# Kernel optimization log

Hardware: AMD Instinct MI355X
Metric: run time of the kernel (lower is better)

Reference implementation:

```python
import jax, jax.numpy as jnp
import numpy as np
import itertools

RANK = 2  # window size per axis; mode='linear' -> stride 1; rank_op='avg'; rank_mode='drop'


def setup_inputs() -> dict:
    key = jax.random.key(0)
    k1, k2, k3 = jax.random.split(key, 3)
    m = 32
    D = 20
    hypervol = jax.random.normal(k1, (D, D, D, D, m), dtype=jnp.float32)
    # nn.Linear weight init U(-0.5, 0.5); P init U(-0.1, 0.1)
    M_w = jax.random.uniform(k2, (m, m), dtype=jnp.float32, minval=-0.5, maxval=0.5)
    P = jax.random.uniform(k3, (m, m), dtype=jnp.float32, minval=-0.1, maxval=0.1)
    return {"hypervol": hypervol, "M_w": M_w, "P": P}


def reference(hypervol, M_w, P):
    m = P.shape[0]
    D1, D2, D3, D4, _ = hypervol.shape
    o1, o2, o3, o4 = D1 - RANK + 1, D2 - RANK + 1, D3 - RANK + 1, D4 - RANK + 1

    # Vectorized window extraction with mean reduction ('avg'):
    # mean over RANK^4 window = average of RANK^4 shifted slices (fixed small loop).
    acc = jnp.zeros((o1, o2, o3, o4, m), dtype=hypervol.dtype)
    for a, b, c, d in itertools.product(range(RANK), repeat=4):
        acc = acc + hypervol[a:a + o1, b:b + o2, c:c + o3, d:d + o4, :]
    win = acc / float(RANK ** 4)  # [o1,o2,o3,o4,m]

    # M(v): Linear without bias -> v @ W^T
    x = jnp.einsum('abcdj,ij->abcdi', win, M_w)  # [o1,o2,o3,o4,m]
    # note: output index of Linear is i; below x plays role of (M v) with einsum index j
    x = jnp.einsum('abcdi->abcdi', x)  # no-op, keep shape clear

    # periods[i,j] = i*m + j + 2 (identical for all four axes)
    ii = jnp.arange(m, dtype=jnp.float32)
    periods = ii[:, None] * m + ii[None, :] + 2.0  # [m,m]
    two_pi = jnp.float32(2.0 * np.pi)

    def ctab(n):
        k = jnp.arange(n, dtype=jnp.float32)
        return jnp.cos(two_pi * k[:, None, None] / periods)  # [n,m,m]

    C1, C2, C3, C4 = ctab(o1), ctab(o2), ctab(o3), ctab(o4)
    # phi[a,b,c,d,i,j] = C1[a]*C2[b]*C3[c]*C4[d]; built from tiny per-axis tables
    phi = (C1[:, None, None, None] * C2[None, :, None, None]) \
          [:, :, :, None] * 0.0  # placeholder removed below
    phi = (C1[:, None, None, None, :, :]
           * C2[None, :, None, None, :, :]
           * C3[None, None, :, None, :, :]
           * C4[None, None, None, :, :, :])  # [o1,o2,o3,o4,m,m]

    # N(k)_i = sum_j P_ij * (Mv)_j * phi_ij  (matches einsum 'bj,ij,bij->bi')
    Nk = jnp.einsum('abcdj,ij,abcdij->abcdi', x, P, phi)
    return Nk.reshape(-1, m)  # [num_windows, m], window order = k1-major like the loops
```

## Files before the change

kernel.cpp:

```cpp
#include <hip/hip_runtime.h>

#define DD 20
#define MM 32
#define OO 19
#define NBLK (OO*OO*OO)

#define CT_FLOATS (OO*MM*MM)
#define PT_OFF CT_FLOATS
#define MT_OFF (PT_OFF + MM*MM)
#define WS_FLOATS (MT_OFF + MM*MM)

__global__ __launch_bounds__(256) void build_tables_kernel(
        const float* __restrict__ Mw, const float* __restrict__ P,
        float* __restrict__ ws) {
    int idx = blockIdx.x * 256 + threadIdx.x;
    if (idx < CT_FLOATS) {
        int k = idx >> 10;
        int r = idx & 1023;
        int j = r >> 5;
        int i = r & 31;
        float period = (float)(i * MM + j + 2);
        ws[idx] = cosf(6.28318530717958647692f * (float)k / period);
    } else if (idx < MT_OFF) {
        int r = idx - PT_OFF;
        ws[idx] = P[(r & 31) * MM + (r >> 5)];
    } else if (idx < WS_FLOATS) {
        int r = idx - MT_OFF;
        ws[idx] = Mw[(r & 31) * MM + (r >> 5)];
    }
}

__global__ __launch_bounds__(256) void spatial_kernel(
        const float* __restrict__ H, const float* __restrict__ ws,
        float* __restrict__ out) {
    __shared__ float sS[DD * MM];
    __shared__ float sMt[MM * MM];
    __shared__ float sQPt[MM * MM];
    __shared__ float sX[OO * MM];

    const int tid = threadIdx.x;
    const int i = tid & 31;
    const int g = tid >> 5;

    const int blk = blockIdx.x;
    const int c = blk % OO;
    const int b = (blk / OO) % OO;
    const int a = blk / (OO * OO);

    const float* __restrict__ Ct = ws;
    const float* __restrict__ Pt = ws + PT_OFF;
    const float* __restrict__ Mt = ws + MT_OFF;

    ((float4*)sMt)[tid] = ((const float4*)Mt)[tid];

    {
        float4 p  = ((const float4*)Pt)[tid];
        float4 xa = ((const float4*)(Ct + a * (MM*MM)))[tid];
        float4 xb = ((const float4*)(Ct + b * (MM*MM)))[tid];
        float4 xc = ((const float4*)(Ct + c * (MM*MM)))[tid];
        float4 q;
        q.x = p.x * xa.x * xb.x * xc.x;
        q.y = p.y * xa.y * xb.y * xc.y;
        q.z = p.z * xa.z * xb.z * xc.z;
        q.w = p.w * xa.w * xb.w * xc.w;
        ((float4*)sQPt)[tid] = q;
    }

    for (int d = g; d < DD; d += 8) {
        float s = 0.f;
        #pragma unroll
        for (int da = 0; da < 2; ++da)
            #pragma unroll
            for (int db = 0; db < 2; ++db)
                #pragma unroll
                for (int dc = 0; dc < 2; ++dc) {
                    int base = (((a + da) * DD + (b + db)) * DD + (c + dc)) * DD + d;
                    s += H[base * MM + i];
                }
        sS[d * MM + i] = s;
    }
    __syncthreads();

    for (int d = g; d < OO; d += 8) {
        float acc = 0.f;
        #pragma unroll
        for (int j = 0; j < MM; ++j) {
            float wj = (sS[d * MM + j] + sS[(d + 1) * MM + j]) * 0.0625f;
            acc += wj * sMt[j * MM + i];
        }
        sX[d * MM + i] = acc;
    }
    __syncthreads();

    for (int d = g; d < OO; d += 8) {
        float xr[MM];
        #pragma unroll
        for (int jj = 0; jj < MM / 4; ++jj) {
            float4 v = ((const float4*)(sX + d * MM))[jj];
            xr[jj*4+0] = v.x; xr[jj*4+1] = v.y; xr[jj*4+2] = v.z; xr[jj*4+3] = v.w;
        }
        const float* __restrict__ ctd = Ct + d * (MM*MM) + i;
        float acc = 0.f;
        #pragma unroll
        for (int j = 0; j < MM; ++j) {
            acc += xr[j] * sQPt[j * MM + i] * ctd[j * MM];
        }
        out[(blk * OO + d) * MM + i] = acc;
    }
}

extern "C" void kernel_launch(void* const* d_in, const int* in_sizes, int n_in,
                              void* d_out, int out_size, void* d_ws, size_t ws_size,
                              hipStream_t stream) {
    const float* H  = (const float*)d_in[0];
    const float* Mw = (const float*)d_in[1];
    const float* P  = (const float*)d_in[2];
    float* out = (float*)d_out;
    float* ws  = (float*)d_ws;

    const int tblocks = (WS_FLOATS + 255) / 256;
    build_tables_kernel<<<tblocks, 256, 0, stream>>>(Mw, P, ws);
    spatial_kernel<<<NBLK, 256, 0, stream>>>(H, ws, out);
}
```

Measured before the change: 112.8 us.

## Register-tile two outputs per thread, vectorize loads, and remap blocks per XCD

Each thread now computes two output channels across a contiguous range of d rows. The per-block P·Ca·Cb·Cc product is held in registers as float2 instead of shared memory. Window sums use float4 loads from H, the averaged row is staged once in a padded shared buffer, and block IDs are remapped so neighbouring blocks land on the same XCD for better L2 reuse of overlapping H slices. The trade is higher register pressure (64 floats for qp plus 32 for xr) and an uneven d split across thread groups (2 rows for g<3, 1 otherwise).

```diff
diff --git a/kernel.cpp b/kernel.cpp
--- a/kernel.cpp
+++ b/kernel.cpp
@@ -9,6 +9,8 @@
 #define PT_OFF CT_FLOATS
 #define MT_OFF (PT_OFF + MM*MM)
 #define WS_FLOATS (MT_OFF + MM*MM)
+
+#define SWS 36
 
 __global__ __launch_bounds__(256) void build_tables_kernel(
         const float* __restrict__ Mw, const float* __restrict__ P,
@@ -34,15 +36,21 @@
         const float* __restrict__ H, const float* __restrict__ ws,
         float* __restrict__ out) {
     __shared__ float sS[DD * MM];
+    __shared__ float sW[OO * SWS];
+    __shared__ float sX[OO * SWS];
     __shared__ float sMt[MM * MM];
-    __shared__ float sQPt[MM * MM];
-    __shared__ float sX[OO * MM];
 
     const int tid = threadIdx.x;
-    const int i = tid & 31;
-    const int g = tid >> 5;
+    const int i2  = tid & 15;
+    const int i   = i2 * 2;
+    const int g   = tid >> 4;
+    const int d0  = (g < 3) ? (2 * g) : (g + 3);
+    const int d1  = d0 + ((g < 3) ? 2 : 1);
 
-    const int blk = blockIdx.x;
+    const int raw = blockIdx.x;
+    const int xcd = raw & 7;
+    const int k   = raw >> 3;
+    const int blk = (xcd < 3) ? (xcd * 858 + k) : (2574 + (xcd - 3) * 857 + k);
     const int c = blk % OO;
     const int b = (blk / OO) % OO;
     const int a = blk / (OO * OO);
@@ -53,59 +61,80 @@
 
     ((float4*)sMt)[tid] = ((const float4*)Mt)[tid];
 
+    float2 qp[MM];
     {
-        float4 p  = ((const float4*)Pt)[tid];
-        float4 xa = ((const float4*)(Ct + a * (MM*MM)))[tid];
-        float4 xb = ((const float4*)(Ct + b * (MM*MM)))[tid];
-        float4 xc = ((const float4*)(Ct + c * (MM*MM)))[tid];
-        float4 q;
-        q.x = p.x * xa.x * xb.x * xc.x;
-        q.y = p.y * xa.y * xb.y * xc.y;
-        q.z = p.z * xa.z * xb.z * xc.z;
-        q.w = p.w * xa.w * xb.w * xc.w;
-        ((float4*)sQPt)[tid] = q;
+        const float2* p  = (const float2*)(Pt + i);
+        const float2* ca = (const float2*)(Ct + a * (MM * MM) + i);
+        const float2* cb = (const float2*)(Ct + b * (MM * MM) + i);
+        const float2* cc = (const float2*)(Ct + c * (MM * MM) + i);
+        #pragma unroll
+        for (int j = 0; j < MM; ++j) {
+            float2 pv = p[j * 16];
+            float2 va = ca[j * 16];
+            float2 vb = cb[j * 16];
+            float2 vc = cc[j * 16];
+            qp[j].x = pv.x * va.x * vb.x * vc.x;
+            qp[j].y = pv.y * va.y * vb.y * vc.y;
+        }
     }
 
-    for (int d = g; d < DD; d += 8) {
-        float s = 0.f;
-        #pragma unroll
-        for (int da = 0; da < 2; ++da)
+    {
+        const int dd = tid >> 3;
+        const int q  = tid & 7;
+        if (dd < DD) {
+            float4 s = make_float4(0.f, 0.f, 0.f, 0.f);
             #pragma unroll
-            for (int db = 0; db < 2; ++db)
+            for (int da = 0; da < 2; ++da)
                 #pragma unroll
-                for (int dc = 0; dc < 2; ++dc) {
-                    int base = (((a + da) * DD + (b + db)) * DD + (c + dc)) * DD + d;
-                    s += H[base * MM + i];
-                }
-        sS[d * MM + i] = s;
+                for (int db = 0; db < 2; ++db)
+                    #pragma unroll
+                    for (int dc = 0; dc < 2; ++dc) {
+                        const float4 v = *(const float4*)(
+                            H + (size_t)((((a + da) * DD + (b + db)) * DD + (c + dc)) * DD + dd) * MM + q * 4);
+                        s.x += v.x; s.y += v.y; s.z += v.z; s.w += v.w;
+                    }
+            ((float4*)(sS + dd * MM))[q] = s;
+        }
     }
     __syncthreads();
 
-    for (int d = g; d < OO; d += 8) {
-        float acc = 0.f;
-        #pragma unroll
-        for (int j = 0; j < MM; ++j) {
-            float wj = (sS[d * MM + j] + sS[(d + 1) * MM + j]) * 0.0625f;
-            acc += wj * sMt[j * MM + i];
-        }
-        sX[d * MM + i] = acc;
+    for (int idx = tid; idx < OO * MM; idx += 256) {
+        const int d = idx >> 5, j = idx & 31;
+        sW[d * SWS + j] = (sS[d * MM + j] + sS[d * MM + MM + j]) * 0.0625f;
     }
     __syncthreads();
 
-    for (int d = g; d < OO; d += 8) {
+    for (int d = d0; d < d1; ++d) {
+        float2 acc = make_float2(0.f, 0.f);
+        #pragma unroll
+        for (int j = 0; j < MM; ++j) {
+            const float wj = sW[d * SWS + j];
+            const float2 mt = *(const float2*)(sMt + j * MM + i);
+            acc.x += wj * mt.x;
+            acc.y += wj * mt.y;
+        }
+        *(float2*)(sX + d * SWS + i) = acc;
+    }
+    __syncthreads();
+
+    for (int d = d0; d < d1; ++d) {
         float xr[MM];
         #pragma unroll
         for (int jj = 0; jj < MM / 4; ++jj) {
-            float4 v = ((const float4*)(sX + d * MM))[jj];
-            xr[jj*4+0] = v.x; xr[jj*4+1] = v.y; xr[jj*4+2] = v.z; xr[jj*4+3] = v.w;
+            const float4 v = ((const float4*)(sX + d * SWS))[jj];
+            xr[jj * 4 + 0] = v.x; xr[jj * 4 + 1] = v.y;
+            xr[jj * 4 + 2] = v.z; xr[jj * 4 + 3] = v.w;
         }
-        const float* __restrict__ ctd = Ct + d * (MM*MM) + i;
-        float acc = 0.f;
+        const float* __restrict__ ctd = Ct + d * (MM * MM) + i;
+        float2 acc = make_float2(0.f, 0.f);
         #pragma unroll
         for (int j = 0; j < MM; ++j) {
-            acc += xr[j] * sQPt[j * MM + i] * ctd[j * MM];
+            const float2 ct = *(const float2*)(ctd + j * MM);
+            const float t = xr[j];
+            acc.x += t * qp[j].x * ct.x;
+            acc.y += t * qp[j].y * ct.y;
         }
-        out[(blk * OO + d) * MM + i] = acc;
+        *(float2*)(out + (size_t)(blk * OO + d) * MM + i) = acc;
     }
 }
 
```

New measurement: 375.3 us. 233% more time.

## Process four windows per block, one per wavefront, with Chebyshev cosine recurrence

Applied to the files above, without the earlier changes.

Each 64-lane wavefront now handles one (a,b,c) window independently, so block barriers become wave-level syncs. H is loaded as float2 vectors, the Linear weights are held in registers, and the j-reduction is split across the two half-waves and combined with a shuffle. The per-d cosine table is no longer loaded; cos(k*theta) is produced by the Chebyshev recurrence 2cos*prev - prevprev, which can let float rounding error build up over the 19 steps. The block-to-window mapping is also remapped to spread work across the XCDs.

```diff
diff --git a/kernel.cpp b/kernel.cpp
--- a/kernel.cpp
+++ b/kernel.cpp
@@ -3,7 +3,9 @@
 #define DD 20
 #define MM 32
 #define OO 19
-#define NBLK (OO*OO*OO)
+#define NWIN (OO*OO*OO)
+#define WPB 4
+#define NBLK ((NWIN + WPB - 1) / WPB)
 
 #define CT_FLOATS (OO*MM*MM)
 #define PT_OFF CT_FLOATS
@@ -30,82 +32,132 @@
     }
 }
 
-__global__ __launch_bounds__(256) void spatial_kernel(
+__device__ __forceinline__ void wave_sync() {
+    __builtin_amdgcn_s_waitcnt(0);
+    __builtin_amdgcn_wave_barrier();
+}
+
+__global__ __launch_bounds__(256, 4) void spatial_kernel(
         const float* __restrict__ H, const float* __restrict__ ws,
         float* __restrict__ out) {
-    __shared__ float sS[DD * MM];
-    __shared__ float sMt[MM * MM];
-    __shared__ float sQPt[MM * MM];
-    __shared__ float sX[OO * MM];
+    __shared__ __align__(16) float sS[WPB][DD * MM];
+    __shared__ __align__(16) float sW[WPB][OO * MM];
+    __shared__ __align__(16) float sX[WPB][OO * MM];
 
-    const int tid = threadIdx.x;
-    const int i = tid & 31;
-    const int g = tid >> 5;
+    const int tid  = threadIdx.x;
+    const int w    = tid >> 6;
+    const int lane = tid & 63;
+    const int i    = lane & 31;
+    const int h    = lane >> 5;
+    const int jb   = h * 16;
 
-    const int blk = blockIdx.x;
-    const int c = blk % OO;
-    const int b = (blk / OO) % OO;
-    const int a = blk / (OO * OO);
+    const int raw = blockIdx.x;
+    const int xcd = raw & 7;
+    const int k   = raw >> 3;
+    const int sb  = (xcd < 3) ? (xcd * 215 + k) : (645 + (xcd - 3) * 214 + k);
+    const int win = sb * WPB + w;
+    if (win >= NWIN) return;
+    const int c = win % OO;
+    const int b = (win / OO) % OO;
+    const int a = win / (OO * OO);
 
     const float* __restrict__ Ct = ws;
     const float* __restrict__ Pt = ws + PT_OFF;
     const float* __restrict__ Mt = ws + MT_OFF;
 
-    ((float4*)sMt)[tid] = ((const float4*)Mt)[tid];
+    float* __restrict__ S = sS[w];
+    float* __restrict__ W = sW[w];
+    float* __restrict__ X = sX[w];
 
     {
-        float4 p  = ((const float4*)Pt)[tid];
-        float4 xa = ((const float4*)(Ct + a * (MM*MM)))[tid];
-        float4 xb = ((const float4*)(Ct + b * (MM*MM)))[tid];
-        float4 xc = ((const float4*)(Ct + c * (MM*MM)))[tid];
-        float4 q;
-        q.x = p.x * xa.x * xb.x * xc.x;
-        q.y = p.y * xa.y * xb.y * xc.y;
-        q.z = p.z * xa.z * xb.z * xc.z;
-        q.w = p.w * xa.w * xb.w * xc.w;
-        ((float4*)sQPt)[tid] = q;
-    }
-
-    for (int d = g; d < DD; d += 8) {
-        float s = 0.f;
+        float2 acc[5];
+        #pragma unroll
+        for (int kk = 0; kk < 5; ++kk) acc[kk] = make_float2(0.f, 0.f);
         #pragma unroll
         for (int da = 0; da < 2; ++da)
             #pragma unroll
             for (int db = 0; db < 2; ++db)
                 #pragma unroll
                 for (int dc = 0; dc < 2; ++dc) {
-                    int base = (((a + da) * DD + (b + db)) * DD + (c + dc)) * DD + d;
-                    s += H[base * MM + i];
+                    const float2* __restrict__ p = (const float2*)(
+                        H + (size_t)((((a + da) * DD + (b + db)) * DD + (c + dc)) * DD) * MM);
+                    #pragma unroll
+                    for (int kk = 0; kk < 5; ++kk) {
+                        const float2 v = p[kk * 64 + lane];
+                        acc[kk].x += v.x; acc[kk].y += v.y;
+                    }
                 }
-        sS[d * MM + i] = s;
+        #pragma unroll
+        for (int kk = 0; kk < 5; ++kk)
+            ((float2*)S)[kk * 64 + lane] = acc[kk];
     }
-    __syncthreads();
+    wave_sync();
 
-    for (int d = g; d < OO; d += 8) {
-        float acc = 0.f;
+    #pragma unroll
+    for (int t = 0; t < 10; ++t) {
+        const int idx = t * 64 + lane;
+        if (idx < OO * MM)
+            W[idx] = (S[idx] + S[idx + MM]) * 0.0625f;
+    }
+    wave_sync();
+
+    {
+        float mt[16];
         #pragma unroll
-        for (int j = 0; j < MM; ++j) {
-            float wj = (sS[d * MM + j] + sS[(d + 1) * MM + j]) * 0.0625f;
-            acc += wj * sMt[j * MM + i];
+        for (int jj = 0; jj < 16; ++jj)
+            mt[jj] = Mt[(jb + jj) * MM + i];
+
+        #pragma unroll
+        for (int d = 0; d < OO; ++d) {
+            const float4* __restrict__ wr = (const float4*)(W + d * MM + jb);
+            float t = 0.f;
+            #pragma unroll
+            for (int q = 0; q < 4; ++q) {
+                const float4 v = wr[q];
+                t += v.x * mt[q*4+0] + v.y * mt[q*4+1]
+                   + v.z * mt[q*4+2] + v.w * mt[q*4+3];
+            }
+            t += __shfl_xor(t, 32, 64);
+            if (h == 0) X[d * MM + i] = t;
         }
-        sX[d * MM + i] = acc;
     }
-    __syncthreads();
+    wave_sync();
 
-    for (int d = g; d < OO; d += 8) {
-        float xr[MM];
+    float s0[16], s1[16], t2c[16];
+    {
+        const float* __restrict__ cta = Ct + a * (MM * MM);
+        const float* __restrict__ ctb = Ct + b * (MM * MM);
+        const float* __restrict__ ctc = Ct + c * (MM * MM);
+        const float* __restrict__ ct1 = Ct + 1 * (MM * MM);
         #pragma unroll
-        for (int jj = 0; jj < MM / 4; ++jj) {
-            float4 v = ((const float4*)(sX + d * MM))[jj];
-            xr[jj*4+0] = v.x; xr[jj*4+1] = v.y; xr[jj*4+2] = v.z; xr[jj*4+3] = v.w;
+        for (int jj = 0; jj < 16; ++jj) {
+            const int o = (jb + jj) * MM + i;
+            const float qp  = Pt[o] * cta[o] * ctb[o] * ctc[o];
+            const float cw  = ct1[o];
+            t2c[jj] = cw + cw;
+            s1[jj]  = qp;
+            s0[jj]  = qp * cw;
         }
-        const float* __restrict__ ctd = Ct + d * (MM*MM) + i;
-        float acc = 0.f;
+    }
+    const size_t obase = (size_t)win * (OO * MM);
+    #pragma unroll
+    for (int d = 0; d < OO; ++d) {
+        const float4* __restrict__ xr = (const float4*)(X + d * MM + jb);
+        float t = 0.f;
         #pragma unroll
-        for (int j = 0; j < MM; ++j) {
-            acc += xr[j] * sQPt[j * MM + i] * ctd[j * MM];
+        for (int q = 0; q < 4; ++q) {
+            const float4 v = xr[q];
+            t += v.x * s1[q*4+0] + v.y * s1[q*4+1]
+               + v.z * s1[q*4+2] + v.w * s1[q*4+3];
         }
-        out[(blk * OO + d) * MM + i] = acc;
+        #pragma unroll
+        for (int jj = 0; jj < 16; ++jj) {
+            const float nx = __builtin_fmaf(t2c[jj], s1[jj], -s0[jj]);
+            s0[jj] = s1[jj];
+            s1[jj] = nx;
+        }
+        t += __shfl_xor(t, 32, 64);
+        if (h == 0) out[obase + d * MM + i] = t;
     }
 }
 
```

Measured after the change: 94.78 us. 16.0% less time.
